# Optimization experiments

Hardware: AMD Instinct MI355X
Metric: run time of the kernel (lower is better)

Reference implementation:

```python
import jax, jax.numpy as jnp
import numpy as np

B = 4
P0, P1, P2 = 196608, 49152, 12288
DEG = 8
K = 4
EPS = 1e-5


def _cheb_conv(x, cols, vals, W, b):
    """Chebyshev graph conv. x: (B,P,Cin); cols/vals: (P,DEG) fixed-degree sparse L;
    W: (K*Cin, Cout); b: (Cout,). Recursion: T0=x, T1=Lx, Tk=2 L T_{k-1} - T_{k-2}."""
    def lmul(y):  # sparse matvec per batch/channel: (B,P,C) -> (B,P,C)
        return jnp.einsum('pd,bpdc->bpc', vals, y[:, cols, :])
    t0 = x
    t1 = lmul(t0)
    terms = [t0, t1]
    for _ in range(K - 2):
        t2 = 2.0 * lmul(t1) - t0
        terms.append(t2)
        t0, t1 = t1, t2
    xk = jnp.concatenate(terms, axis=-1)  # (B,P,K*Cin)
    return xk @ W + b


def _layernorm(h, g, bt):
    mu = jnp.mean(h, axis=-1, keepdims=True)
    var = jnp.mean(jnp.square(h - mu), axis=-1, keepdims=True)
    return g * (h - mu) / jnp.sqrt(var + EPS) + bt


def _avg_pool4(h):  # HEALPix nested-order average pooling: (B,P,C) -> (B,P//4,C)
    Bh, P, C = h.shape
    return h.reshape(Bh, P // 4, 4, C).mean(axis=2)


def setup_inputs() -> dict:
    key = jax.random.key(0)
    ks = jax.random.split(key, 16)
    cin, c1, c2, c3 = 16, 64, 128, 256
    hid, emb = 512, 256

    def glorot(k, shape):
        fan_in = shape[0]
        return jax.random.normal(k, shape, jnp.float32) / np.sqrt(fan_in)

    inp = {
        'x': jax.random.normal(ks[0], (B, P0, cin), jnp.float32),
        'cols1': jax.random.randint(ks[1], (P0, DEG), 0, P0),
        'vals1': 0.2 * jax.random.normal(ks[2], (P0, DEG), jnp.float32),
        'cols2': jax.random.randint(ks[3], (P1, DEG), 0, P1),
        'vals2': 0.2 * jax.random.normal(ks[4], (P1, DEG), jnp.float32),
        'cols3': jax.random.randint(ks[5], (P2, DEG), 0, P2),
        'vals3': 0.2 * jax.random.normal(ks[6], (P2, DEG), jnp.float32),
        'W1': glorot(ks[7], (K * cin, c1)), 'b1': jnp.zeros((c1,), jnp.float32),
        'g1': jnp.ones((c1,), jnp.float32), 'bt1': jnp.zeros((c1,), jnp.float32),
        'W2': glorot(ks[8], (K * c1, c2)), 'b2': jnp.zeros((c2,), jnp.float32),
        'g2': jnp.ones((c2,), jnp.float32), 'bt2': jnp.zeros((c2,), jnp.float32),
        'W3': glorot(ks[9], (K * c2, c3)), 'b3': jnp.zeros((c3,), jnp.float32),
        'g3': jnp.ones((c3,), jnp.float32), 'bt3': jnp.zeros((c3,), jnp.float32),
        'mW1': glorot(ks[10], (c3, hid)), 'mb1': jnp.zeros((hid,), jnp.float32),
        'mW2': glorot(ks[11], (hid, emb)), 'mb2': jnp.zeros((emb,), jnp.float32),
    }
    return inp


def reference(x, cols1, vals1, cols2, vals2, cols3, vals3,
              W1, b1, g1, bt1, W2, b2, g2, bt2, W3, b3, g3, bt3,
              mW1, mb1, mW2, mb2):
    # Stage 1: ChebConv -> LayerNorm -> ReLU -> avg pool (4:1)
    h = _cheb_conv(x, cols1, vals1, W1, b1)
    h = jax.nn.relu(_layernorm(h, g1, bt1))
    h = _avg_pool4(h)
    # Stage 2
    h = _cheb_conv(h, cols2, vals2, W2, b2)
    h = jax.nn.relu(_layernorm(h, g2, bt2))
    h = _avg_pool4(h)
    # Stage 3 (last stage: no pooling)
    h = _cheb_conv(h, cols3, vals3, W3, b3)
    h = jax.nn.relu(_layernorm(h, g3, bt3))
    # Global mean pool over pixels, then MLP head (Linear-ReLU-Linear)
    z = h.mean(axis=1)                     # (B, 256)
    z = jax.nn.relu(z @ mW1 + mb1)
    z = z @ mW2 + mb2                      # (B, 256)
    return z
```

## Files before the change

kernel.cpp:

```cpp
#include <hip/hip_runtime.h>
#include <hip/hip_bf16.h>

namespace {

constexpr int B  = 4;
constexpr int P0 = 196608, P1 = 49152, P2 = 12288;
constexpr int DEG = 8;
constexpr float EPS = 1e-5f;
constexpr int NBLK3 = (P2 * B) / 64;
constexpr int RSL = 16;
constexpr int RPB = NBLK3 / RSL;

typedef __attribute__((ext_vector_type(4))) float f32x4;
typedef __attribute__((ext_vector_type(8))) short s16x8;

__device__ __forceinline__ float b2f(unsigned short u) {
    union { unsigned int i; float f; } c; c.i = (unsigned int)u << 16; return c.f;
}
__device__ __forceinline__ unsigned short f2b(float f) {
    __hip_bfloat16 h = __float2bfloat16(f);
    return *reinterpret_cast<unsigned short*>(&h);
}

__global__ __launch_bounds__(256)
void x2p_kernel(const float* __restrict__ in, unsigned short* __restrict__ out)
{
    long idx = (long)blockIdx.x * blockDim.x + threadIdx.x;
    if (idx >= (long)P0 * B * 2) return;
    int  h = (int)(idx & 1);
    int  b = (int)((idx >> 1) & 3);
    long p = idx >> 3;
    const float* src = in + ((size_t)b * P0 + p) * 16 + h * 8;
    float4 v0 = *(const float4*)src;
    float4 v1 = *(const float4*)(src + 4);
    union { uint4 u; unsigned short s[8]; } o;
    o.s[0] = f2b(v0.x); o.s[1] = f2b(v0.y); o.s[2] = f2b(v0.z); o.s[3] = f2b(v0.w);
    o.s[4] = f2b(v1.x); o.s[5] = f2b(v1.y); o.s[6] = f2b(v1.z); o.s[7] = f2b(v1.w);
    *(uint4*)&out[((size_t)p * B + b) * 16 + h * 8] = o.u;
}

__global__ __launch_bounds__(256)
void wt_all_kernel(const float* __restrict__ W1, const float* __restrict__ W2,
                   const float* __restrict__ W3,
                   unsigned short* __restrict__ Wt1, unsigned short* __restrict__ Wt2,
                   unsigned short* __restrict__ Wt3)
{
    int i = blockIdx.x * 256 + threadIdx.x;
    if (i < 4096) {
        int n = i % 64, k = i / 64;
        Wt1[n * 64 + k] = f2b(W1[i]);
    } else if (i < 4096 + 32768) {
        int j = i - 4096;
        int n = j % 128, k = j / 128;
        Wt2[n * 256 + k] = f2b(W2[j]);
    } else if (i < 4096 + 32768 + 131072) {
        int j = i - 36864;
        int n = j % 256, k = j / 256;
        Wt3[n * 512 + k] = f2b(W3[j]);
    }
}

template <int CV8>
__global__ __launch_bounds__(256)
void lmul_v2_kernel(const unsigned short* __restrict__ in,
                    const unsigned short* __restrict__ prev,
                    const int* __restrict__ cols, const float* __restrict__ vals,
                    unsigned short* __restrict__ out,
                    float alpha, float beta)
{
    constexpr int ROWS = 256 / CV8;
    __shared__ int   cs[ROWS * DEG];
    __shared__ float vs[ROWS * DEG];
    const int tid = threadIdx.x;
    const long r0 = (long)blockIdx.x * ROWS;
    if (tid < ROWS * DEG) {
        cs[tid] = cols[r0 * DEG + tid];
        vs[tid] = vals[r0 * DEG + tid];
    }
    __syncthreads();

    const int v  = tid & (CV8 - 1);
    const int lr = tid / CV8;
    const uint4* in16 = (const uint4*)in;

    float acc[8] = {0.f,0.f,0.f,0.f,0.f,0.f,0.f,0.f};
#pragma unroll
    for (int d = 0; d < DEG; ++d) {
        int   col = cs[lr * DEG + d];
        float w   = vs[lr * DEG + d];
        union { uint4 u; unsigned short s[8]; } x;
        x.u = in16[(size_t)col * CV8 + v];
#pragma unroll
        for (int j = 0; j < 8; ++j) acc[j] = fmaf(w, b2f(x.s[j]), acc[j]);
    }
    size_t o = (size_t)(r0 + lr) * CV8 + v;
    if (beta != 0.f) {
        union { uint4 u; unsigned short s[8]; } pv;
        pv.u = ((const uint4*)prev)[o];
#pragma unroll
        for (int j = 0; j < 8; ++j)
            acc[j] = fmaf(alpha, acc[j], beta * b2f(pv.s[j]));
    } else if (alpha != 1.f) {
#pragma unroll
        for (int j = 0; j < 8; ++j) acc[j] *= alpha;
    }
    union { uint4 u; unsigned short s[8]; } ou;
#pragma unroll
    for (int j = 0; j < 8; ++j) ou.s[j] = f2b(acc[j]);
    ((uint4*)out)[o] = ou.u;
}

__global__ __launch_bounds__(256)
void s1_mm_kernel(const unsigned short* __restrict__ t0,
                  const unsigned short* __restrict__ t1,
                  const unsigned short* __restrict__ t2,
                  const unsigned short* __restrict__ t3,
                  const unsigned short* __restrict__ Wt,
                  const float* __restrict__ bias,
                  const float* __restrict__ gam,
                  const float* __restrict__ bet,
                  unsigned short* __restrict__ out)
{
    const int wave = threadIdx.x >> 6;
    const int lane = threadIdx.x & 63;
    const int g    = lane >> 4;
    const int c16  = lane & 15;

    s16x8 wf[2][4];
#pragma unroll
    for (int ks = 0; ks < 2; ++ks)
#pragma unroll
        for (int n = 0; n < 4; ++n)
            wf[ks][n] = *(const s16x8*)&Wt[(size_t)(n * 16 + c16) * 64 + ks * 32 + g * 8];

    float bz[4], gz[4], tz[4];
#pragma unroll
    for (int n = 0; n < 4; ++n) {
        bz[n] = bias[n * 16 + c16];
        gz[n] = gam [n * 16 + c16];
        tz[n] = bet [n * 16 + c16];
    }

    const unsigned short* tb[4] = { t0, t1, t2, t3 };
    const int term0  = g >> 1;
    const int coloff = (g & 1) * 8;
    const int bb     = c16 >> 2;
    const int px     = c16 & 3;

    constexpr int NT = P0 / 4;
    const int wg     = blockIdx.x * 4 + wave;
    const int wstep  = gridDim.x * 4;

    for (int t = wg; t < NT; t += wstep) {
        size_t rowbase = ((size_t)(t * 4 + px) * 4 + bb) * 16 + coloff;
        s16x8 a0 = *(const s16x8*)&tb[term0    ][rowbase];
        s16x8 a1 = *(const s16x8*)&tb[term0 + 2][rowbase];

        f32x4 acc[4];
#pragma unroll
        for (int n = 0; n < 4; ++n) acc[n] = (f32x4){bz[n], bz[n], bz[n], bz[n]};
#pragma unroll
        for (int n = 0; n < 4; ++n)
            acc[n] = __builtin_amdgcn_mfma_f32_16x16x32_bf16(a0, wf[0][n], acc[n], 0, 0, 0);
#pragma unroll
        for (int n = 0; n < 4; ++n)
            acc[n] = __builtin_amdgcn_mfma_f32_16x16x32_bf16(a1, wf[1][n], acc[n], 0, 0, 0);

        float s[4] = {0,0,0,0}, q[4] = {0,0,0,0};
#pragma unroll
        for (int n = 0; n < 4; ++n)
#pragma unroll
            for (int r = 0; r < 4; ++r) {
                float v = acc[n][r];
                s[r] += v; q[r] += v * v;
            }
#pragma unroll
        for (int msk = 1; msk < 16; msk <<= 1)
#pragma unroll
            for (int r = 0; r < 4; ++r) {
                s[r] += __shfl_xor(s[r], msk, 64);
                q[r] += __shfl_xor(q[r], msk, 64);
            }
        float mu[4], rs[4];
#pragma unroll
        for (int r = 0; r < 4; ++r) {
            mu[r] = s[r] * (1.f / 64.f);
            float var = q[r] * (1.f / 64.f) - mu[r] * mu[r];
            rs[r] = rsqrtf(var + EPS);
        }
        size_t ro = ((size_t)t * 4 + g) * 64;
#pragma unroll
        for (int n = 0; n < 4; ++n) {
            float pv = 0.f;
#pragma unroll
            for (int r = 0; r < 4; ++r) {
                float h = fmaf(gz[n] * rs[r], acc[n][r] - mu[r], tz[n]);
                pv += fmaxf(h, 0.f);
            }
            out[ro + n * 16 + c16] = f2b(pv * 0.25f);
        }
    }
}

template <int CIN, int COUT, int POOL, int LOG2CIN>
__global__ __launch_bounds__(256)
void cheb_mm_v2_kernel(const unsigned short* __restrict__ t0,
                       const unsigned short* __restrict__ t1,
                       const unsigned short* __restrict__ t2,
                       const unsigned short* __restrict__ t3,
                       const unsigned short* __restrict__ Wt,
                       const float* __restrict__ bias,
                       const float* __restrict__ gam,
                       const float* __restrict__ bet,
                       void* __restrict__ outv)
{
    constexpr int KC   = 4 * CIN;
    constexpr int WNF  = COUT / 64;
    constexpr int NKCH = KC / 64;
    constexpr int LDA  = 72;

    __shared__ unsigned short As[64 * LDA];
    __shared__ unsigned short Ws[COUT * LDA];
    __shared__ float sq[64][4][2];

    const int tid  = threadIdx.x;
    const int wave = tid >> 6;
    const int lane = tid & 63;
    const int g    = lane >> 4;
    const int c16  = lane & 15;
    const int wcol = wave * (COUT / 4);

    const unsigned short* tb[4] = { t0, t1, t2, t3 };

    float bz[WNF], gz[WNF], tz[WNF];
#pragma unroll
    for (int n = 0; n < WNF; ++n) {
        bz[n] = bias[wcol + n * 16 + c16];
        gz[n] = gam [wcol + n * 16 + c16];
        tz[n] = bet [wcol + n * 16 + c16];
    }

    f32x4 acc[4][WNF];
#pragma unroll
    for (int m = 0; m < 4; ++m)
#pragma unroll
        for (int n = 0; n < WNF; ++n)
            acc[m][n] = (f32x4){bz[n], bz[n], bz[n], bz[n]};

    for (int kc = 0; kc < NKCH; ++kc) {
        if (kc) __syncthreads();
#pragma unroll
        for (int i = tid; i < 64 * 8; i += 256) {
            int row = i >> 3, v = i & 7;
            int k = kc * 64 + v * 8;
            int term = k >> LOG2CIN;
            int c = k & (CIN - 1);
            size_t srow;
            if constexpr (POOL == 4) {
                int pix = blockIdx.x * 16 + ((row >> 4) << 2) + (row & 3);
                int rb  = (row >> 2) & 3;
                srow = ((size_t)pix * B + rb) * CIN + c;
            } else {
                srow = ((size_t)(blockIdx.x * 64 + row)) * CIN + c;
            }
            *(uint4*)&As[row * LDA + v * 8] = *(const uint4*)&tb[term][srow];
        }
#pragma unroll
        for (int i = tid; i < COUT * 8; i += 256) {
            int co = i >> 3, v = i & 7;
            *(uint4*)&Ws[co * LDA + v * 8] =
                *(const uint4*)&Wt[(size_t)co * KC + kc * 64 + v * 8];
        }
        __syncthreads();
#pragma unroll
        for (int ks = 0; ks < 2; ++ks) {
            s16x8 a[4];
#pragma unroll
            for (int m = 0; m < 4; ++m)
                a[m] = *(const s16x8*)&As[(m * 16 + c16) * LDA + ks * 32 + g * 8];
#pragma unroll
            for (int n = 0; n < WNF; ++n) {
                s16x8 bf = *(const s16x8*)&Ws[(wcol + n * 16 + c16) * LDA + ks * 32 + g * 8];
#pragma unroll
                for (int m = 0; m < 4; ++m)
                    acc[m][n] = __builtin_amdgcn_mfma_f32_16x16x32_bf16(a[m], bf, acc[m][n], 0, 0, 0);
            }
        }
    }

    float sm[4][4], qm[4][4];
#pragma unroll
    for (int m = 0; m < 4; ++m)
#pragma unroll
        for (int r = 0; r < 4; ++r) { sm[m][r] = 0.f; qm[m][r] = 0.f; }
#pragma unroll
    for (int m = 0; m < 4; ++m)
#pragma unroll
        for (int n = 0; n < WNF; ++n)
#pragma unroll
            for (int r = 0; r < 4; ++r) {
                float v = acc[m][n][r];
                sm[m][r] += v; qm[m][r] += v * v;
            }
#pragma unroll
    for (int msk = 1; msk < 16; msk <<= 1)
#pragma unroll
        for (int m = 0; m < 4; ++m)
#pragma unroll
            for (int r = 0; r < 4; ++r) {
                sm[m][r] += __shfl_xor(sm[m][r], msk, 64);
                qm[m][r] += __shfl_xor(qm[m][r], msk, 64);
            }
    __syncthreads();
    if (c16 == 0) {
#pragma unroll
        for (int m = 0; m < 4; ++m)
#pragma unroll
            for (int r = 0; r < 4; ++r) {
                sq[m * 16 + g * 4 + r][wave][0] = sm[m][r];
                sq[m * 16 + g * 4 + r][wave][1] = qm[m][r];
            }
    }
    __syncthreads();
    float mu[4][4], rs[4][4];
#pragma unroll
    for (int m = 0; m < 4; ++m)
#pragma unroll
        for (int r = 0; r < 4; ++r) {
            int row = m * 16 + g * 4 + r;
            float ss = sq[row][0][0] + sq[row][1][0] + sq[row][2][0] + sq[row][3][0];
            float qq = sq[row][0][1] + sq[row][1][1] + sq[row][2][1] + sq[row][3][1];
            mu[m][r] = ss * (1.f / COUT);
            float var = qq * (1.f / COUT) - mu[m][r] * mu[m][r];
            rs[m][r] = rsqrtf(var + EPS);
        }

    if constexpr (POOL == 4) {
        unsigned short* out = (unsigned short*)outv;
#pragma unroll
        for (int m = 0; m < 4; ++m) {
            size_t ro = ((size_t)(blockIdx.x * 4 + m) * B + g) * COUT + wcol;
#pragma unroll
            for (int n = 0; n < WNF; ++n) {
                float pv = 0.f;
#pragma unroll
                for (int r = 0; r < 4; ++r) {
                    float h = fmaf(gz[n] * rs[m][r], acc[m][n][r] - mu[m][r], tz[n]);
                    pv += fmaxf(h, 0.f);
                }
                out[ro + n * 16 + c16] = f2b(pv * 0.25f);
            }
        }
    } else {
        float part[WNF][4];
#pragma unroll
        for (int n = 0; n < WNF; ++n)
#pragma unroll
            for (int r = 0; r < 4; ++r) part[n][r] = 0.f;
#pragma unroll
        for (int m = 0; m < 4; ++m)
#pragma unroll
            for (int n = 0; n < WNF; ++n)
#pragma unroll
                for (int r = 0; r < 4; ++r) {
                    float h = fmaf(gz[n] * rs[m][r], acc[m][n][r] - mu[m][r], tz[n]);
                    part[n][r] += fmaxf(h, 0.f);
                }
#pragma unroll
        for (int n = 0; n < WNF; ++n)
#pragma unroll
            for (int r = 0; r < 4; ++r) {
                part[n][r] += __shfl_xor(part[n][r], 16, 64);
                part[n][r] += __shfl_xor(part[n][r], 32, 64);
            }
        if (g == 0) {
            float* zb = (float*)outv + (size_t)blockIdx.x * B * COUT;
#pragma unroll
            for (int n = 0; n < WNF; ++n)
#pragma unroll
                for (int r = 0; r < 4; ++r)
                    zb[(size_t)r * COUT + wcol + n * 16 + c16] = part[n][r];
        }
    }
}

__global__ __launch_bounds__(256)
void zred_kernel(const float* __restrict__ zblk, float* __restrict__ zp2)
{
    int s   = blockIdx.x >> 2;
    int col = (blockIdx.x & 3) * 256 + threadIdx.x;
    float acc = 0.f;
#pragma unroll 8
    for (int r = 0; r < RPB; ++r)
        acc += zblk[(size_t)(s * RPB + r) * (B * 256) + col];
    zp2[(size_t)s * (B * 256) + col] = acc;
}

__global__ __launch_bounds__(512)
void head_kernel(const float* __restrict__ zp2,
                 const float* __restrict__ mW1, const float* __restrict__ mb1,
                 const float* __restrict__ mW2, const float* __restrict__ mb2,
                 float* __restrict__ out)
{
    __shared__ float zs[256];
    __shared__ float hsh[512];
    int b = blockIdx.x, tid = threadIdx.x;
    if (tid < 256) {
        float s = 0.f;
#pragma unroll
        for (int sl = 0; sl < RSL; ++sl)
            s += zp2[(size_t)sl * (B * 256) + b * 256 + tid];
        zs[tid] = s * (1.0f / P2);
    }
    __syncthreads();
    {
        float a = mb1[tid];
#pragma unroll 8
        for (int i = 0; i < 256; ++i) a = fmaf(zs[i], mW1[i * 512 + tid], a);
        hsh[tid] = fmaxf(a, 0.f);
    }
    __syncthreads();
    if (tid < 256) {
        float a = mb2[tid];
#pragma unroll 8
        for (int i = 0; i < 512; ++i) a = fmaf(hsh[i], mW2[i * 256 + tid], a);
        out[(size_t)b * 256 + tid] = a;
    }
}

}

extern "C" void kernel_launch(void* const* d_in, const int* in_sizes, int n_in,
                              void* d_out, int out_size, void* d_ws, size_t ws_size,
                              hipStream_t stream)
{
    const float* x     = (const float*)d_in[0];
    const int*   cols1 = (const int*)  d_in[1];
    const float* vals1 = (const float*)d_in[2];
    const int*   cols2 = (const int*)  d_in[3];
    const float* vals2 = (const float*)d_in[4];
    const int*   cols3 = (const int*)  d_in[5];
    const float* vals3 = (const float*)d_in[6];
    const float* W1  = (const float*)d_in[7];
    const float* b1  = (const float*)d_in[8];
    const float* g1  = (const float*)d_in[9];
    const float* bt1 = (const float*)d_in[10];
    const float* W2  = (const float*)d_in[11];
    const float* b2  = (const float*)d_in[12];
    const float* g2  = (const float*)d_in[13];
    const float* bt2 = (const float*)d_in[14];
    const float* W3  = (const float*)d_in[15];
    const float* b3  = (const float*)d_in[16];
    const float* g3  = (const float*)d_in[17];
    const float* bt3 = (const float*)d_in[18];
    const float* mW1 = (const float*)d_in[19];
    const float* mb1 = (const float*)d_in[20];
    const float* mW2 = (const float*)d_in[21];
    const float* mb2 = (const float*)d_in[22];
    float* out = (float*)d_out;

    char* w = (char*)d_ws;
    size_t off = 0;
    auto alloc = [&](size_t bytes) -> void* {
        void* p = w + off;
        off += (bytes + 255) & ~(size_t)255;
        return p;
    };
    const size_t E1 = (size_t)B * P0 * 16;
    unsigned short* xb  = (unsigned short*)alloc(E1 * 2);
    unsigned short* t_a = (unsigned short*)alloc(E1 * 2);
    unsigned short* t_b = (unsigned short*)alloc(E1 * 2);
    unsigned short* t_c = (unsigned short*)alloc(E1 * 2);
    unsigned short* h1  = (unsigned short*)alloc((size_t)P1 * B * 64 * 2);
    unsigned short* h2  = (unsigned short*)alloc((size_t)P2 * B * 128 * 2);
    unsigned short* Wt1 = (unsigned short*)alloc(64 * 64 * 2);
    unsigned short* Wt2 = (unsigned short*)alloc(256 * 128 * 2);
    unsigned short* Wt3 = (unsigned short*)alloc(512 * 256 * 2);
    float*          zblk = (float*)alloc((size_t)NBLK3 * B * 256 * 4);
    float*          zp2  = (float*)alloc((size_t)RSL * B * 256 * 4);

    x2p_kernel<<<(int)(((long)P0 * B * 2 + 255) / 256), 256, 0, stream>>>(x, xb);
    wt_all_kernel<<<(4096 + 32768 + 131072 + 255) / 256, 256, 0, stream>>>(
        W1, W2, W3, Wt1, Wt2, Wt3);

    {
        lmul_v2_kernel<8><<<P0 / 32, 256, 0, stream>>>(xb,  nullptr, cols1, vals1, t_a, 1.f,  0.f);
        lmul_v2_kernel<8><<<P0 / 32, 256, 0, stream>>>(t_a, xb,      cols1, vals1, t_b, 2.f, -1.f);
        lmul_v2_kernel<8><<<P0 / 32, 256, 0, stream>>>(t_b, t_a,     cols1, vals1, t_c, 2.f, -1.f);
        s1_mm_kernel<<<2048, 256, 0, stream>>>(xb, t_a, t_b, t_c, Wt1, b1, g1, bt1, h1);
    }
    {
        lmul_v2_kernel<32><<<P1 / 8, 256, 0, stream>>>(h1,  nullptr, cols2, vals2, t_a, 1.f,  0.f);
        lmul_v2_kernel<32><<<P1 / 8, 256, 0, stream>>>(t_a, h1,      cols2, vals2, t_b, 2.f, -1.f);
        lmul_v2_kernel<32><<<P1 / 8, 256, 0, stream>>>(t_b, t_a,     cols2, vals2, t_c, 2.f, -1.f);
        cheb_mm_v2_kernel<64, 128, 4, 6><<<(P1 * B) / 64, 256, 0, stream>>>(
            h1, t_a, t_b, t_c, Wt2, b2, g2, bt2, h2);
    }
    {
        lmul_v2_kernel<64><<<P2 / 4, 256, 0, stream>>>(h2,  nullptr, cols3, vals3, t_a, 1.f,  0.f);
        lmul_v2_kernel<64><<<P2 / 4, 256, 0, stream>>>(t_a, h2,      cols3, vals3, t_b, 2.f, -1.f);
        lmul_v2_kernel<64><<<P2 / 4, 256, 0, stream>>>(t_b, t_a,     cols3, vals3, t_c, 2.f, -1.f);
        cheb_mm_v2_kernel<128, 256, 1, 7><<<NBLK3, 256, 0, stream>>>(
            h2, t_a, t_b, t_c, Wt3, b3, g3, bt3, zblk);
    }
    zred_kernel<<<RSL * 4, 256, 0, stream>>>(zblk, zp2);
    head_kernel<<<B, 512, 0, stream>>>(zp2, mW1, mb1, mW2, mb2, out);

    (void)in_sizes; (void)n_in; (void)out_size; (void)ws_size;
}
```

Measured before the change: 438.8 us.

## Enlarge chebconv GEMM tiles to 2D wave grid with XOR-swizzled LDS

```diff
diff --git a/kernel.cpp b/kernel.cpp
--- a/kernel.cpp
+++ b/kernel.cpp
@@ -202,9 +202,9 @@
     }
 }
 
-template <int CIN, int COUT, int POOL, int LOG2CIN>
-__global__ __launch_bounds__(256)
-void cheb_mm_v2_kernel(const unsigned short* __restrict__ t0,
+template <int CIN, int COUT, int GM, int GN, int POOL, int LOG2CIN>
+__global__ __launch_bounds__(512)
+void cheb_mm_v3_kernel(const unsigned short* __restrict__ t0,
                        const unsigned short* __restrict__ t1,
                        const unsigned short* __restrict__ t2,
                        const unsigned short* __restrict__ t3,
@@ -215,76 +215,81 @@
                        void* __restrict__ outv)
 {
     constexpr int KC   = 4 * CIN;
-    constexpr int WNF  = COUT / 64;
+    constexpr int BM   = GM * 64;
     constexpr int NKCH = KC / 64;
-    constexpr int LDA  = 72;
-
-    __shared__ unsigned short As[64 * LDA];
-    __shared__ unsigned short Ws[COUT * LDA];
-    __shared__ float sq[64][4][2];
+
+    __shared__ unsigned short As[BM * 64];
+    __shared__ unsigned short Ws[COUT * 64];
+    __shared__ float sq[BM][GN][2];
 
     const int tid  = threadIdx.x;
-    const int wave = tid >> 6;
+    const int wv   = tid >> 6;
+    const int gm   = wv / GN;
+    const int gn   = wv % GN;
     const int lane = tid & 63;
     const int g    = lane >> 4;
     const int c16  = lane & 15;
-    const int wcol = wave * (COUT / 4);
 
     const unsigned short* tb[4] = { t0, t1, t2, t3 };
 
-    float bz[WNF], gz[WNF], tz[WNF];
-#pragma unroll
-    for (int n = 0; n < WNF; ++n) {
-        bz[n] = bias[wcol + n * 16 + c16];
-        gz[n] = gam [wcol + n * 16 + c16];
-        tz[n] = bet [wcol + n * 16 + c16];
-    }
-
-    f32x4 acc[4][WNF];
+    float bz[4], gz[4], tz[4];
+#pragma unroll
+    for (int n = 0; n < 4; ++n) {
+        int col = gn * 64 + n * 16 + c16;
+        bz[n] = bias[col]; gz[n] = gam[col]; tz[n] = bet[col];
+    }
+
+    f32x4 acc[4][4];
 #pragma unroll
     for (int m = 0; m < 4; ++m)
 #pragma unroll
-        for (int n = 0; n < WNF; ++n)
+        for (int n = 0; n < 4; ++n)
             acc[m][n] = (f32x4){bz[n], bz[n], bz[n], bz[n]};
 
     for (int kc = 0; kc < NKCH; ++kc) {
         if (kc) __syncthreads();
 #pragma unroll
-        for (int i = tid; i < 64 * 8; i += 256) {
+        for (int it = 0; it < BM * 8 / 512; ++it) {
+            int i = tid + it * 512;
             int row = i >> 3, v = i & 7;
             int k = kc * 64 + v * 8;
             int term = k >> LOG2CIN;
             int c = k & (CIN - 1);
             size_t srow;
             if constexpr (POOL == 4) {
-                int pix = blockIdx.x * 16 + ((row >> 4) << 2) + (row & 3);
+                int pix = blockIdx.x * (BM / 4) + ((row >> 4) << 2) + (row & 3);
                 int rb  = (row >> 2) & 3;
                 srow = ((size_t)pix * B + rb) * CIN + c;
             } else {
-                srow = ((size_t)(blockIdx.x * 64 + row)) * CIN + c;
-            }
-            *(uint4*)&As[row * LDA + v * 8] = *(const uint4*)&tb[term][srow];
-        }
-#pragma unroll
-        for (int i = tid; i < COUT * 8; i += 256) {
+                srow = ((size_t)(blockIdx.x * BM + row)) * CIN + c;
+            }
+            *(uint4*)((char*)As + row * 128 + ((v * 16) ^ ((row & 7) << 4))) =
+                *(const uint4*)&tb[term][srow];
+        }
+#pragma unroll
+        for (int it = 0; it < COUT * 8 / 512; ++it) {
+            int i = tid + it * 512;
             int co = i >> 3, v = i & 7;
-            *(uint4*)&Ws[co * LDA + v * 8] =
+            *(uint4*)((char*)Ws + co * 128 + ((v * 16) ^ ((co & 7) << 4))) =
                 *(const uint4*)&Wt[(size_t)co * KC + kc * 64 + v * 8];
         }
         __syncthreads();
 #pragma unroll
         for (int ks = 0; ks < 2; ++ks) {
-            s16x8 a[4];
+            const int cb  = ks * 64 + g * 16;
+            const int swz = cb ^ ((c16 & 7) << 4);
+            s16x8 a[4], bw[4];
 #pragma unroll
             for (int m = 0; m < 4; ++m)
-                a[m] = *(const s16x8*)&As[(m * 16 + c16) * LDA + ks * 32 + g * 8];
-#pragma unroll
-            for (int n = 0; n < WNF; ++n) {
-                s16x8 bf = *(const s16x8*)&Ws[(wcol + n * 16 + c16) * LDA + ks * 32 + g * 8];
+                a[m] = *(const s16x8*)((const char*)As + (gm * 64 + m * 16 + c16) * 128 + swz);
+#pragma unroll
+            for (int n = 0; n < 4; ++n)
+                bw[n] = *(const s16x8*)((const char*)Ws + (gn * 64 + n * 16 + c16) * 128 + swz);
+#pragma unroll
+            for (int n = 0; n < 4; ++n)
 #pragma unroll
                 for (int m = 0; m < 4; ++m)
-                    acc[m][n] = __builtin_amdgcn_mfma_f32_16x16x32_bf16(a[m], bf, acc[m][n], 0, 0, 0);
-            }
+                    acc[m][n] = __builtin_amdgcn_mfma_f32_16x16x32_bf16(a[m], bw[n], acc[m][n], 0, 0, 0);
         }
     }
 
@@ -296,7 +301,7 @@
 #pragma unroll
     for (int m = 0; m < 4; ++m)
 #pragma unroll
-        for (int n = 0; n < WNF; ++n)
+        for (int n = 0; n < 4; ++n)
 #pragma unroll
             for (int r = 0; r < 4; ++r) {
                 float v = acc[m][n][r];
@@ -317,8 +322,8 @@
         for (int m = 0; m < 4; ++m)
 #pragma unroll
             for (int r = 0; r < 4; ++r) {
-                sq[m * 16 + g * 4 + r][wave][0] = sm[m][r];
-                sq[m * 16 + g * 4 + r][wave][1] = qm[m][r];
+                sq[gm * 64 + m * 16 + g * 4 + r][gn][0] = sm[m][r];
+                sq[gm * 64 + m * 16 + g * 4 + r][gn][1] = qm[m][r];
             }
     }
     __syncthreads();
@@ -327,59 +332,60 @@
     for (int m = 0; m < 4; ++m)
 #pragma unroll
         for (int r = 0; r < 4; ++r) {
-            int row = m * 16 + g * 4 + r;
-            float ss = sq[row][0][0] + sq[row][1][0] + sq[row][2][0] + sq[row][3][0];
-            float qq = sq[row][0][1] + sq[row][1][1] + sq[row][2][1] + sq[row][3][1];
+            int row = gm * 64 + m * 16 + g * 4 + r;
+            float ss = 0.f, qq = 0.f;
+#pragma unroll
+            for (int j = 0; j < GN; ++j) { ss += sq[row][j][0]; qq += sq[row][j][1]; }
             mu[m][r] = ss * (1.f / COUT);
             float var = qq * (1.f / COUT) - mu[m][r] * mu[m][r];
             rs[m][r] = rsqrtf(var + EPS);
         }
 
     if constexpr (POOL == 4) {
-        unsigned short* out = (unsigned short*)outv;
+        unsigned short* outp = (unsigned short*)outv;
 #pragma unroll
         for (int m = 0; m < 4; ++m) {
-            size_t ro = ((size_t)(blockIdx.x * 4 + m) * B + g) * COUT + wcol;
-#pragma unroll
-            for (int n = 0; n < WNF; ++n) {
+            size_t ro = ((size_t)(blockIdx.x * (BM / 16) + gm * 4 + m) * B + g) * COUT + gn * 64;
+#pragma unroll
+            for (int n = 0; n < 4; ++n) {
                 float pv = 0.f;
 #pragma unroll
                 for (int r = 0; r < 4; ++r) {
                     float h = fmaf(gz[n] * rs[m][r], acc[m][n][r] - mu[m][r], tz[n]);
                     pv += fmaxf(h, 0.f);
                 }
-                out[ro + n * 16 + c16] = f2b(pv * 0.25f);
+                outp[ro + n * 16 + c16] = f2b(pv * 0.25f);
             }
         }
     } else {
-        float part[WNF][4];
-#pragma unroll
-        for (int n = 0; n < WNF; ++n)
+        float part[4][4];
+#pragma unroll
+        for (int n = 0; n < 4; ++n)
 #pragma unroll
             for (int r = 0; r < 4; ++r) part[n][r] = 0.f;
 #pragma unroll
         for (int m = 0; m < 4; ++m)
 #pragma unroll
-            for (int n = 0; n < WNF; ++n)
+            for (int n = 0; n < 4; ++n)
 #pragma unroll
                 for (int r = 0; r < 4; ++r) {
                     float h = fmaf(gz[n] * rs[m][r], acc[m][n][r] - mu[m][r], tz[n]);
                     part[n][r] += fmaxf(h, 0.f);
                 }
 #pragma unroll
-        for (int n = 0; n < WNF; ++n)
+        for (int n = 0; n < 4; ++n)
 #pragma unroll
             for (int r = 0; r < 4; ++r) {
                 part[n][r] += __shfl_xor(part[n][r], 16, 64);
                 part[n][r] += __shfl_xor(part[n][r], 32, 64);
             }
         if (g == 0) {
-            float* zb = (float*)outv + (size_t)blockIdx.x * B * COUT;
-#pragma unroll
-            for (int n = 0; n < WNF; ++n)
+            float* zb = (float*)outv + ((size_t)(blockIdx.x * GM + gm)) * (B * COUT);
+#pragma unroll
+            for (int n = 0; n < 4; ++n)
 #pragma unroll
                 for (int r = 0; r < 4; ++r)
-                    zb[(size_t)r * COUT + wcol + n * 16 + c16] = part[n][r];
+                    zb[(size_t)r * COUT + gn * 64 + n * 16 + c16] = part[n][r];
         }
     }
 }
@@ -493,14 +499,14 @@
         lmul_v2_kernel<32><<<P1 / 8, 256, 0, stream>>>(h1,  nullptr, cols2, vals2, t_a, 1.f,  0.f);
         lmul_v2_kernel<32><<<P1 / 8, 256, 0, stream>>>(t_a, h1,      cols2, vals2, t_b, 2.f, -1.f);
         lmul_v2_kernel<32><<<P1 / 8, 256, 0, stream>>>(t_b, t_a,     cols2, vals2, t_c, 2.f, -1.f);
-        cheb_mm_v2_kernel<64, 128, 4, 6><<<(P1 * B) / 64, 256, 0, stream>>>(
+        cheb_mm_v3_kernel<64, 128, 4, 2, 4, 6><<<(P1 * B) / 256, 512, 0, stream>>>(
             h1, t_a, t_b, t_c, Wt2, b2, g2, bt2, h2);
     }
     {
         lmul_v2_kernel<64><<<P2 / 4, 256, 0, stream>>>(h2,  nullptr, cols3, vals3, t_a, 1.f,  0.f);
         lmul_v2_kernel<64><<<P2 / 4, 256, 0, stream>>>(t_a, h2,      cols3, vals3, t_b, 2.f, -1.f);
         lmul_v2_kernel<64><<<P2 / 4, 256, 0, stream>>>(t_b, t_a,     cols3, vals3, t_c, 2.f, -1.f);
-        cheb_mm_v2_kernel<128, 256, 1, 7><<<NBLK3, 256, 0, stream>>>(
+        cheb_mm_v3_kernel<128, 256, 2, 4, 1, 7><<<(P2 * B) / 128, 512, 0, stream>>>(
             h2, t_a, t_b, t_c, Wt3, b3, g3, bt3, zblk);
     }
     zred_kernel<<<RSL * 4, 256, 0, stream>>>(zblk, zp2);
```

Result: faster. 420.9 us (-4.1%).
